# Performance work log

Measured on AMD Instinct MI355X. Metric: run time of the kernel, lower is better.

## Reference

```python
import jax, jax.numpy as jnp
from jax import lax
import numpy as np

B, C_IN, H, W = 4, 3, 128, 128
K, D = 8192, 16  # num_embeddings, embedding_size (= encoder out channels)


def _conv(x, w, b):
    # x: (B,C,H,W), w: (O,I,3,3) OIHW, VALID padding, stride 1
    y = lax.conv_general_dilated(x, w, (1, 1), 'VALID',
                                 dimension_numbers=('NCHW', 'OIHW', 'NCHW'))
    return y + b[None, :, None, None]


def _conv_t(x, w, b):
    # transpose conv, stride 1, k=3: correlate with flipped/transposed kernel, pad 2
    # w: (I,O,3,3) -> flip spatial, swap to OIHW
    wk = jnp.flip(w, (2, 3)).transpose(1, 0, 2, 3)
    y = lax.conv_general_dilated(x, wk, (1, 1), [(2, 2), (2, 2)],
                                 dimension_numbers=('NCHW', 'OIHW', 'NCHW'))
    return y + b[None, :, None, None]


def setup_inputs() -> dict:
    key = jax.random.key(0)
    ks = jax.random.split(key, 14)
    g = lambda k, shp, fan: jax.random.normal(k, shp, jnp.float32) / np.float32(np.sqrt(fan))
    return {
        'x':   jax.random.normal(ks[0], (B, C_IN, H, W), jnp.float32),
        'ew1': g(ks[1], (4, C_IN, 3, 3), C_IN * 9), 'eb1': jnp.zeros((4,), jnp.float32),
        'ew2': g(ks[2], (8, 4, 3, 3), 4 * 9),       'eb2': jnp.zeros((8,), jnp.float32),
        'ew3': g(ks[3], (16, 8, 3, 3), 8 * 9),      'eb3': jnp.zeros((16,), jnp.float32),
        'dw1': g(ks[4], (16, 8, 3, 3), 16 * 9),     'db1': jnp.zeros((8,), jnp.float32),
        'dw2': g(ks[5], (8, 4, 3, 3), 8 * 9),       'db2': jnp.zeros((4,), jnp.float32),
        'dw3': g(ks[6], (4, C_IN, 3, 3), 4 * 9),    'db3': jnp.zeros((C_IN,), jnp.float32),
        'codebook': jax.random.normal(ks[7], (K, D), jnp.float32) * 0.02,
    }


def reference(x, ew1, eb1, ew2, eb2, ew3, eb3, dw1, db1, dw2, db2, dw3, db3, codebook):
    # encode
    z = jax.nn.selu(_conv(x, ew1, eb1))
    z = jax.nn.selu(_conv(z, ew2, eb2))
    z = _conv(z, ew3, eb3)                      # (B, D, h, w)
    b, d, h, w = z.shape
    zf = z.transpose(0, 2, 3, 1).reshape(-1, d)  # (N, D) flattened latents
    # ||z - e||^2 = ||z||^2 - 2 z.e + ||e||^2, argmin over codebook rows
    d2 = ((zf * zf).sum(1, keepdims=True)
          - 2.0 * (zf @ codebook.T)
          + (codebook * codebook).sum(1)[None, :])  # (N, K)
    idx = jnp.argmin(d2, axis=1)                 # (N,) int32
    zq = codebook[idx].reshape(b, h, w, d).transpose(0, 3, 1, 2)  # gather + reshape
    # decode
    y = jax.nn.selu(_conv_t(zq, dw1, db1))
    y = jax.nn.selu(_conv_t(y, dw2, db2))
    y = _conv_t(y, dw3, db3)                     # (B, C_IN, H, W)
    return (y, idx)
```

## Files before the change

### kernel.cpp

```cpp
#include <hip/hip_runtime.h>
#include <math.h>

#define BATCH 4
#define DLAT 16
#define KCB 8192
#define HLAT 122
#define PIX (HLAT*HLAT)
#define NLAT (BATCH*PIX)
#define NT32 (KCB/32)
#define ROWSB 32
#define NVQBLK 1861
#define NWAVE 4
#define TW (NT32/NWAVE)
#define CAPW 1024
#define NCONVBLK 3721

typedef _Float16 half8 __attribute__((ext_vector_type(8)));
typedef float f32x16 __attribute__((ext_vector_type(16)));

__device__ __forceinline__ float selu_np(float x) {
    const float scale = 1.0507009873554805f, alpha = 1.6732632423543772f;
    if (x > 0.f) return __fmul_rn(scale, x);
    return __fmul_rn(scale, __fmul_rn(alpha, expm1f(x)));
}

template<int CI, int CO, int HIN, int WIN, bool DOSELU>
__global__ void conv3x3_np(const float* __restrict__ in, const float* __restrict__ w,
                           const float* __restrict__ bias, float* __restrict__ out) {
    constexpr int HO = HIN - 2, WO = WIN - 2;
    int tid = blockIdx.x * blockDim.x + threadIdx.x;
    constexpr int total = BATCH * CO * HO * WO;
    if (tid >= total) return;
    int j = tid % WO; int t = tid / WO;
    int i = t % HO;   t /= HO;
    int o = t % CO;   int b = t / CO;
    float acc = 0.f;
    for (int c = 0; c < CI; ++c) {
        const float* ip = in + ((b * CI + c) * HIN + i) * WIN + j;
        const float* wp = w + ((o * CI + c) * 3) * 3;
        #pragma unroll
        for (int p = 0; p < 3; ++p)
            #pragma unroll
            for (int q = 0; q < 3; ++q)
                acc = __fmaf_rn(ip[p * WIN + q], wp[p * 3 + q], acc);
    }
    acc = __fadd_rn(acc, bias[o]);
    out[tid] = DOSELU ? selu_np(acc) : acc;
}

__global__ void conv3_last_np(const float* __restrict__ in, const float* __restrict__ w,
                              const float* __restrict__ bias, float* __restrict__ zf,
                              _Float16* __restrict__ zh, float* __restrict__ blockmax) {
    constexpr int CI = 8, HIN = 124, WIN = 124, WO = 122;
    __shared__ float sred[4];
    int tid = blockIdx.x * 256 + threadIdx.x;
    int o  = tid & 15;
    int pp = tid >> 4;
    int b = pp / PIX, pix = pp % PIX;
    int i = pix / WO, j = pix % WO;
    float acc = 0.f;
    for (int c = 0; c < CI; ++c) {
        const float* ip = in + ((b * CI + c) * HIN + i) * WIN + j;
        const float* wp = w + ((o * CI + c) * 3) * 3;
        #pragma unroll
        for (int p = 0; p < 3; ++p)
            #pragma unroll
            for (int q = 0; q < 3; ++q)
                acc = __fmaf_rn(ip[p * WIN + q], wp[p * 3 + q], acc);
    }
    acc = __fadd_rn(acc, bias[o]);
    zf[tid] = acc;
    zh[tid] = (_Float16)acc;
    float m = fabsf(acc);
    #pragma unroll
    for (int off = 32; off; off >>= 1) m = fmaxf(m, __shfl_xor(m, off));
    if ((threadIdx.x & 63) == 0) sred[threadIdx.x >> 6] = m;
    __syncthreads();
    if (threadIdx.x == 0)
        blockmax[blockIdx.x] = fmaxf(fmaxf(sred[0], sred[1]), fmaxf(sred[2], sred[3]));
}

__global__ void reduce_zmax(const float* __restrict__ bm, unsigned* __restrict__ scal) {
    __shared__ float sred[4];
    float m = 0.f;
    for (int i = threadIdx.x; i < NCONVBLK; i += 256) m = fmaxf(m, bm[i]);
    #pragma unroll
    for (int off = 32; off; off >>= 1) m = fmaxf(m, __shfl_xor(m, off));
    if ((threadIdx.x & 63) == 0) sred[threadIdx.x >> 6] = m;
    __syncthreads();
    if (threadIdx.x == 0)
        scal[0] = __float_as_uint(fmaxf(fmaxf(sred[0], sred[1]), fmaxf(sred[2], sred[3])));
}

__device__ __forceinline__ float pairwise16_sq(const float* v) {
    float a[16];
    #pragma unroll
    for (int d = 0; d < 16; ++d) a[d] = __fmul_rn(v[d], v[d]);
    float r0 = __fadd_rn(a[0], a[8]),  r1 = __fadd_rn(a[1], a[9]);
    float r2 = __fadd_rn(a[2], a[10]), r3 = __fadd_rn(a[3], a[11]);
    float r4 = __fadd_rn(a[4], a[12]), r5 = __fadd_rn(a[5], a[13]);
    float r6 = __fadd_rn(a[6], a[14]), r7 = __fadd_rn(a[7], a[15]);
    return __fadd_rn(__fadd_rn(__fadd_rn(r0, r1), __fadd_rn(r2, r3)),
                     __fadd_rn(__fadd_rn(r4, r5), __fadd_rn(r6, r7)));
}

__device__ __forceinline__ void load16(const float* __restrict__ p, float* v) {
    const float4* r = (const float4*)p;
    float4 v0 = r[0], v1 = r[1], v2 = r[2], v3 = r[3];
    v[0]=v0.x; v[1]=v0.y; v[2]=v0.z; v[3]=v0.w;
    v[4]=v1.x; v[5]=v1.y; v[6]=v1.z; v[7]=v1.w;
    v[8]=v2.x; v[9]=v2.y; v[10]=v2.z; v[11]=v2.w;
    v[12]=v3.x; v[13]=v3.y; v[14]=v3.z; v[15]=v3.w;
}

__device__ __forceinline__ float np_d2(const float* zr, float A, const float* e16, float cnk) {
    float g = 0.f;
    #pragma unroll
    for (int d = 0; d < 16; ++d) g = __fmaf_rn(zr[d], e16[d], g);
    return __fadd_rn(__fmaf_rn(-2.f, g, A), cnk);
}

__global__ void init_scal(unsigned* scal) { scal[0] = 0u; scal[1] = 0u; }

__global__ void cbprep(const float* __restrict__ cb, float* __restrict__ cn,
                       _Float16* __restrict__ cbB, unsigned* __restrict__ scal) {
    int k = blockIdx.x * 256 + threadIdx.x;
    float v[16];
    load16(cb + (size_t)k * DLAT, v);
    float C = pairwise16_sq(v);
    cn[k] = C;
    float m = C;
    #pragma unroll
    for (int off = 32; off; off >>= 1) m = fmaxf(m, __shfl_xor(m, off));
    if ((threadIdx.x & 63) == 0) atomicMax(&scal[1], __float_as_uint(m));
    int tile = k >> 5, col = k & 31;
    #pragma unroll
    for (int d = 0; d < 16; ++d) {
        int ln = (d >> 3) * 32 + col;
        cbB[(size_t)tile * 512 + ln * 8 + (d & 7)] = (_Float16)v[d];
    }
}

#define DROW(reg, lanehi) (((reg) & 3) + 8 * ((reg) >> 2) + 4 * (lanehi))

__global__ __launch_bounds__(256, 4) void vq_mfma(
        const _Float16* __restrict__ zh, const float* __restrict__ zf,
        const _Float16* __restrict__ cbB, const float* __restrict__ cn,
        const float* __restrict__ cb, const unsigned* __restrict__ scal,
        float* __restrict__ idx_out, float* __restrict__ zq) {
    __shared__ unsigned list[CAPW];
    __shared__ float resd[CAPW];
    __shared__ float smin[NWAVE][ROWSB];
    __shared__ unsigned lcnt;
    const int tid = threadIdx.x;
    const int w = tid >> 6, lane = tid & 63;
    const int lanehi = lane >> 5;
    const int R0 = blockIdx.x * ROWSB;
    const f32x16 zero16 = {0.f,0.f,0.f,0.f,0.f,0.f,0.f,0.f,0.f,0.f,0.f,0.f,0.f,0.f,0.f,0.f};
    if (tid == 0) lcnt = 0;

    int ar = R0 + (lane & 31);
    if (ar >= NLAT) ar = NLAT - 1;
    half8 a = *(const half8*)(zh + (size_t)ar * DLAT + lanehi * 8);

    float zmaxf = __uint_as_float(scal[0]);
    float en    = sqrtf(__uint_as_float(scal[1]));
    float errG  = 4.f * zmaxf * en * 9.765625e-4f * 1.03f
                + 6.104e-5f * (16.f * zmaxf + 4.f * en);
    float slack = (16.f * zmaxf * zmaxf + 8.f * zmaxf * en + en * en) * 1.2e-7f;
    float DELTA = 4.f * errG + 2.f * slack + 1e-6f;

    const int t0 = w * TW, t1 = t0 + TW;

    float m[16];
    #pragma unroll
    for (int r = 0; r < 16; ++r) m[r] = INFINITY;

    #pragma unroll 2
    for (int t = t0; t < t1; ++t) {
        half8 b = *(const half8*)(cbB + (size_t)t * 512 + lane * 8);
        float cnv = cn[t * 32 + (lane & 31)];
        f32x16 D = __builtin_amdgcn_mfma_f32_32x32x16_f16(a, b, zero16, 0, 0, 0);
        #pragma unroll
        for (int r = 0; r < 16; ++r)
            m[r] = fminf(m[r], __fmaf_rn(-2.f, D[r], cnv));
    }
    #pragma unroll
    for (int r = 0; r < 16; ++r) {
        float v = m[r];
        v = fminf(v, __shfl_xor(v, 1));
        v = fminf(v, __shfl_xor(v, 2));
        v = fminf(v, __shfl_xor(v, 4));
        v = fminf(v, __shfl_xor(v, 8));
        v = fminf(v, __shfl_xor(v, 16));
        m[r] = v;
    }
    if ((lane & 31) == 0) {
        #pragma unroll
        for (int r = 0; r < 16; ++r)
            smin[w][DROW(r, lanehi)] = m[r];
    }
    __syncthreads();
    #pragma unroll
    for (int r = 0; r < 16; ++r) {
        int row = DROW(r, lanehi);
        float v = INFINITY;
        #pragma unroll
        for (int ww = 0; ww < NWAVE; ++ww) v = fminf(v, smin[ww][row]);
        m[r] = v + DELTA;
    }

    #pragma unroll 2
    for (int t = t0; t < t1; ++t) {
        half8 b = *(const half8*)(cbB + (size_t)t * 512 + lane * 8);
        float cnv = cn[t * 32 + (lane & 31)];
        f32x16 D = __builtin_amdgcn_mfma_f32_32x32x16_f16(a, b, zero16, 0, 0, 0);
        bool anyp = false;
        #pragma unroll
        for (int r = 0; r < 16; ++r)
            anyp |= (__fmaf_rn(-2.f, D[r], cnv) <= m[r]);
        if (__ballot(anyp)) {
            #pragma unroll
            for (int r = 0; r < 16; ++r) {
                bool pred = (__fmaf_rn(-2.f, D[r], cnv) <= m[r]);
                unsigned long long bal = __ballot(pred);
                if (bal) {
                    unsigned nb = (unsigned)__popcll(bal);
                    unsigned base = 0;
                    if (lane == 0) base = atomicAdd(&lcnt, nb);
                    base = __shfl(base, 0);
                    unsigned pos = base + (unsigned)__popcll(bal & ((1ull << lane) - 1ull));
                    if (pred && pos < CAPW) {
                        unsigned rs = (unsigned)DROW(r, lanehi);
                        list[pos] = (rs << 13) | (unsigned)(t * 32 + (lane & 31));
                    }
                }
            }
        }
    }
    __syncthreads();
    unsigned cnt = lcnt;

    if (cnt <= CAPW) {
        for (unsigned i = tid; i < cnt; i += 256) {
            unsigned e = list[i];
            int n = R0 + (int)(e >> 13);
            if (n >= NLAT) n = NLAT - 1;
            int k = (int)(e & 8191);
            float zr[16], e16[16];
            load16(zf + (size_t)n * DLAT, zr);
            float A = pairwise16_sq(zr);
            load16(cb + (size_t)k * DLAT, e16);
            resd[i] = np_d2(zr, A, e16, cn[k]);
        }
    }
    __syncthreads();

    if (tid < ROWSB) {
        int r = R0 + tid;
        if (r < NLAT) {
            float bd = INFINITY; int bk = 0x7fffffff;
            if (cnt <= CAPW) {
                for (unsigned i = 0; i < cnt; ++i) {
                    unsigned e = list[i];
                    if ((int)(e >> 13) == tid) {
                        float d2 = resd[i]; int k = (int)(e & 8191);
                        if (d2 < bd || (d2 == bd && k < bk)) { bd = d2; bk = k; }
                    }
                }
            } else {
                float zr[16];
                load16(zf + (size_t)r * DLAT, zr);
                float A = pairwise16_sq(zr);
                for (int k = 0; k < KCB; ++k) {
                    float e16[16];
                    load16(cb + (size_t)k * DLAT, e16);
                    float d2 = np_d2(zr, A, e16, cn[k]);
                    if (d2 < bd) { bd = d2; bk = k; }
                }
            }
            idx_out[r] = (float)bk;
            int b = r / PIX, pix = r % PIX;
            const float* e = cb + (size_t)bk * DLAT;
            #pragma unroll
            for (int d = 0; d < DLAT; ++d) zq[((size_t)(b * DLAT + d)) * PIX + pix] = e[d];
        }
    }
}

template<int CI, int CO, int HIN, int WIN, bool DOSELU>
__global__ void convt3x3(const float* __restrict__ in, const float* __restrict__ w,
                         const float* __restrict__ bias, float* __restrict__ out) {
    constexpr int HO = HIN + 2, WO = WIN + 2;
    int tid = blockIdx.x * blockDim.x + threadIdx.x;
    constexpr int total = BATCH * CO * HO * WO;
    if (tid >= total) return;
    int j = tid % WO; int t = tid / WO;
    int i = t % HO;   t /= HO;
    int o = t % CO;   int b = t / CO;
    float acc = bias[o];
    for (int c = 0; c < CI; ++c) {
        const float* ip = in + ((b * CI + c) * HIN) * WIN;
        const float* wp = w + ((c * CO + o) * 3) * 3;
        #pragma unroll
        for (int p = 0; p < 3; ++p) {
            int ii = i + p - 2;
            if (ii < 0 || ii >= HIN) continue;
            #pragma unroll
            for (int q = 0; q < 3; ++q) {
                int jj = j + q - 2;
                if (jj < 0 || jj >= WIN) continue;
                acc += ip[ii * WIN + jj] * wp[(2 - p) * 3 + (2 - q)];
            }
        }
    }
    const float scale = 1.0507009873554805f, alpha = 1.6732632423543772f;
    out[tid] = DOSELU ? (acc > 0.f ? scale * acc : scale * alpha * (expf(acc) - 1.f)) : acc;
}

extern "C" void kernel_launch(void* const* d_in, const int* in_sizes, int n_in,
                              void* d_out, int out_size, void* d_ws, size_t ws_size,
                              hipStream_t stream) {
    const float* x   = (const float*)d_in[0];
    const float* ew1 = (const float*)d_in[1];  const float* eb1 = (const float*)d_in[2];
    const float* ew2 = (const float*)d_in[3];  const float* eb2 = (const float*)d_in[4];
    const float* ew3 = (const float*)d_in[5];  const float* eb3 = (const float*)d_in[6];
    const float* dw1 = (const float*)d_in[7];  const float* db1 = (const float*)d_in[8];
    const float* dw2 = (const float*)d_in[9];  const float* db2 = (const float*)d_in[10];
    const float* dw3 = (const float*)d_in[11]; const float* db3 = (const float*)d_in[12];
    const float* cb  = (const float*)d_in[13];

    float* out_y   = (float*)d_out;
    float* out_idx = (float*)d_out + 196608;

    float*     ws   = (float*)d_ws;
    float*     zf   = ws;
    float*     e1   = ws + 952576;
    float*     e2   = ws + 1206592;
    float*     fZq  = ws + 952576;
    float*     fB   = ws + 1905152;
    float*     fA   = ws + 2397184;
    _Float16*  zh   = (_Float16*)(ws + 2651200);
    _Float16*  cbB  = (_Float16*)(ws + 3127488);
    float*     cn   = ws + 3193024;
    unsigned*  scal = (unsigned*)(ws + 3201216);
    float*     bmax = ws + 3201218;

    const int TPB = 256;

    init_scal<<<1, 1, 0, stream>>>(scal);

    conv3x3_np<3, 4, 128, 128, true ><<<993,  TPB, 0, stream>>>(x,  ew1, eb1, e1);
    conv3x3_np<4, 8, 126, 126, true ><<<1922, TPB, 0, stream>>>(e1, ew2, eb2, e2);
    conv3_last_np<<<NCONVBLK, TPB, 0, stream>>>(e2, ew3, eb3, zf, zh, bmax);
    reduce_zmax<<<1, TPB, 0, stream>>>(bmax, scal);

    cbprep<<<32, TPB, 0, stream>>>(cb, cn, cbB, scal);
    vq_mfma<<<NVQBLK, TPB, 0, stream>>>(zh, zf, cbB, cn, cb, scal, out_idx, fZq);

    convt3x3<16, 8, 122, 122, true ><<<1922, TPB, 0, stream>>>(fZq, dw1, db1, fB);
    convt3x3<8, 4, 124, 124, true ><<<993,  TPB, 0, stream>>>(fB,  dw2, db2, fA);
    convt3x3<4, 3, 126, 126, false><<<768,  TPB, 0, stream>>>(fA,  dw3, db3, out_y);
}
```

Baseline: 227.1 us.

## Replace second MFMA pass with per-lane minimum candidate rescoring

Drops the second full pass over the codebook that recomputed MFMA distances to gather candidates. Each lane now keeps its own per-row minimum across its strided codebook subset. Lanes whose minimum falls within the row-minimum-plus-DELTA band are recorded in a small per-wave list. For each entry, all 64 lanes rescore the matching codebook column exactly and do a wave argmin reduction. This halves the MFMA work but changes the candidate set: only each lane's own minimum is kept, so other near-ties in that lane's subset may be missed, and any wave overflow falls back to the brute-force path.

New measurement: 287.7 us. 26.7% more time.

```diff
diff --git a/kernel.cpp b/kernel.cpp
--- a/kernel.cpp
+++ b/kernel.cpp
@@ -12,7 +12,8 @@
 #define NVQBLK 1861
 #define NWAVE 4
 #define TW (NT32/NWAVE)
-#define CAPW 1024
+#define CAPW 256
+#define TCAP 64
 #define NCONVBLK 3721
 
 typedef _Float16 half8 __attribute__((ext_vector_type(8)));
@@ -151,6 +152,7 @@
     __shared__ unsigned list[CAPW];
     __shared__ float resd[CAPW];
     __shared__ float smin[NWAVE][ROWSB];
+    __shared__ unsigned tlist[NWAVE][TCAP];
     __shared__ unsigned lcnt;
     const int tid = threadIdx.x;
     const int w = tid >> 6, lane = tid & 63;
@@ -185,6 +187,9 @@
         for (int r = 0; r < 16; ++r)
             m[r] = fminf(m[r], __fmaf_rn(-2.f, D[r], cnv));
     }
+    float mlane[16];
+    #pragma unroll
+    for (int r = 0; r < 16; ++r) mlane[r] = m[r];
     #pragma unroll
     for (int r = 0; r < 16; ++r) {
         float v = m[r];
@@ -210,51 +215,48 @@
         m[r] = v + DELTA;
     }
 
-    #pragma unroll 2
-    for (int t = t0; t < t1; ++t) {
-        half8 b = *(const half8*)(cbB + (size_t)t * 512 + lane * 8);
-        float cnv = cn[t * 32 + (lane & 31)];
-        f32x16 D = __builtin_amdgcn_mfma_f32_32x32x16_f16(a, b, zero16, 0, 0, 0);
-        bool anyp = false;
-        #pragma unroll
-        for (int r = 0; r < 16; ++r)
-            anyp |= (__fmaf_rn(-2.f, D[r], cnv) <= m[r]);
-        if (__ballot(anyp)) {
-            #pragma unroll
-            for (int r = 0; r < 16; ++r) {
-                bool pred = (__fmaf_rn(-2.f, D[r], cnv) <= m[r]);
-                unsigned long long bal = __ballot(pred);
-                if (bal) {
-                    unsigned nb = (unsigned)__popcll(bal);
-                    unsigned base = 0;
-                    if (lane == 0) base = atomicAdd(&lcnt, nb);
-                    base = __shfl(base, 0);
-                    unsigned pos = base + (unsigned)__popcll(bal & ((1ull << lane) - 1ull));
-                    if (pred && pos < CAPW) {
-                        unsigned rs = (unsigned)DROW(r, lanehi);
-                        list[pos] = (rs << 13) | (unsigned)(t * 32 + (lane & 31));
-                    }
-                }
+    unsigned cnt_w = 0;
+    #pragma unroll
+    for (int r = 0; r < 16; ++r) {
+        bool q = (mlane[r] <= m[r]);
+        unsigned long long bal = __ballot(q);
+        if (bal) {
+            unsigned pos = cnt_w + (unsigned)__popcll(bal & ((1ull << lane) - 1ull));
+            if (q && pos < TCAP)
+                tlist[w][pos] = (unsigned)((DROW(r, lanehi) << 5) | (lane & 31));
+            cnt_w += (unsigned)__popcll(bal);
+        }
+    }
+    bool ovf = (cnt_w > TCAP);
+    if (ovf && lane == 0) atomicAdd(&lcnt, CAPW + 1u);
+
+    if (!ovf) {
+        for (unsigned i = 0; i < cnt_w; ++i) {
+            unsigned e = tlist[w][i];
+            int row = (int)(e >> 5), col = (int)(e & 31);
+            int rg = R0 + row; if (rg >= NLAT) rg = NLAT - 1;
+            float zr[16];
+            load16(zf + (size_t)rg * DLAT, zr);
+            float A = pairwise16_sq(zr);
+            int k = (t0 + lane) * 32 + col;
+            float e16[16];
+            load16(cb + (size_t)k * DLAT, e16);
+            float d2 = np_d2(zr, A, e16, cn[k]);
+            int kk = k;
+            #pragma unroll
+            for (int off = 1; off < 64; off <<= 1) {
+                float od = __shfl_xor(d2, off);
+                int   ok = __shfl_xor(kk, off);
+                if (od < d2 || (od == d2 && ok < kk)) { d2 = od; kk = ok; }
+            }
+            if (lane == 0) {
+                unsigned p = atomicAdd(&lcnt, 1u);
+                if (p < CAPW) { list[p] = ((unsigned)row << 13) | (unsigned)kk; resd[p] = d2; }
             }
         }
     }
     __syncthreads();
     unsigned cnt = lcnt;
-
-    if (cnt <= CAPW) {
-        for (unsigned i = tid; i < cnt; i += 256) {
-            unsigned e = list[i];
-            int n = R0 + (int)(e >> 13);
-            if (n >= NLAT) n = NLAT - 1;
-            int k = (int)(e & 8191);
-            float zr[16], e16[16];
-            load16(zf + (size_t)n * DLAT, zr);
-            float A = pairwise16_sq(zr);
-            load16(cb + (size_t)k * DLAT, e16);
-            resd[i] = np_d2(zr, A, e16, cn[k]);
-        }
-    }
-    __syncthreads();
 
     if (tid < ROWSB) {
         int r = R0 + tid;
```

## Stage codebook tiles in LDS with double buffering, 128 rows per VQ block

Applied to the files above, without the earlier changes.

The VQ kernel now gives each wave its own 32 latent rows, so a block covers 128 rows and the grid shrinks about fourfold. Every wave walks the full codebook, which is staged through double-buffered shared memory in chunks of 8 tiles, so each global codebook load is shared by four waves. The cross-wave min reduction in shared memory is gone, and the init_scal launch is folded into reduce_zmax. In exchange each wave does four times as many MFMAs per block, a barrier is added per chunk, occupancy is lowered to 3 blocks per CU, and the 1024-entry candidate list now serves 128 rows instead of 32, so it may overflow into the fallback path more often.

Result: slower. 331.1 us (+45.8%).

```diff
diff --git a/kernel.cpp b/kernel.cpp
--- a/kernel.cpp
+++ b/kernel.cpp
@@ -8,10 +8,11 @@
 #define PIX (HLAT*HLAT)
 #define NLAT (BATCH*PIX)
 #define NT32 (KCB/32)
-#define ROWSB 32
-#define NVQBLK 1861
+#define ROWSB 128
+#define NVQBLK 466
 #define NWAVE 4
-#define TW (NT32/NWAVE)
+#define CHT 8
+#define NCH (NT32/CHT)
 #define CAPW 1024
 #define NCONVBLK 3721
 
@@ -90,6 +91,7 @@
     __syncthreads();
     if (threadIdx.x == 0)
         scal[0] = __float_as_uint(fmaxf(fmaxf(sred[0], sred[1]), fmaxf(sred[2], sred[3])));
+    if (threadIdx.x == 1) scal[1] = 0u;
 }
 
 __device__ __forceinline__ float pairwise16_sq(const float* v) {
@@ -119,8 +121,6 @@
     for (int d = 0; d < 16; ++d) g = __fmaf_rn(zr[d], e16[d], g);
     return __fadd_rn(__fmaf_rn(-2.f, g, A), cnk);
 }
-
-__global__ void init_scal(unsigned* scal) { scal[0] = 0u; scal[1] = 0u; }
 
 __global__ void cbprep(const float* __restrict__ cb, float* __restrict__ cn,
                        _Float16* __restrict__ cbB, unsigned* __restrict__ scal) {
@@ -143,14 +143,14 @@
 
 #define DROW(reg, lanehi) (((reg) & 3) + 8 * ((reg) >> 2) + 4 * (lanehi))
 
-__global__ __launch_bounds__(256, 4) void vq_mfma(
+__global__ __launch_bounds__(256, 3) void vq_mfma(
         const _Float16* __restrict__ zh, const float* __restrict__ zf,
         const _Float16* __restrict__ cbB, const float* __restrict__ cn,
         const float* __restrict__ cb, const unsigned* __restrict__ scal,
         float* __restrict__ idx_out, float* __restrict__ zq) {
+    __shared__ _Float16 sb[2][CHT * 512];
     __shared__ unsigned list[CAPW];
     __shared__ float resd[CAPW];
-    __shared__ float smin[NWAVE][ROWSB];
     __shared__ unsigned lcnt;
     const int tid = threadIdx.x;
     const int w = tid >> 6, lane = tid & 63;
@@ -159,7 +159,7 @@
     const f32x16 zero16 = {0.f,0.f,0.f,0.f,0.f,0.f,0.f,0.f,0.f,0.f,0.f,0.f,0.f,0.f,0.f,0.f};
     if (tid == 0) lcnt = 0;
 
-    int ar = R0 + (lane & 31);
+    int ar = R0 + w * 32 + (lane & 31);
     if (ar >= NLAT) ar = NLAT - 1;
     half8 a = *(const half8*)(zh + (size_t)ar * DLAT + lanehi * 8);
 
@@ -170,71 +170,102 @@
     float slack = (16.f * zmaxf * zmaxf + 8.f * zmaxf * en + en * en) * 1.2e-7f;
     float DELTA = 4.f * errG + 2.f * slack + 1e-6f;
 
-    const int t0 = w * TW, t1 = t0 + TW;
-
-    float m[16];
-    #pragma unroll
-    for (int r = 0; r < 16; ++r) m[r] = INFINITY;
-
-    #pragma unroll 2
-    for (int t = t0; t < t1; ++t) {
-        half8 b = *(const half8*)(cbB + (size_t)t * 512 + lane * 8);
-        float cnv = cn[t * 32 + (lane & 31)];
-        f32x16 D = __builtin_amdgcn_mfma_f32_32x32x16_f16(a, b, zero16, 0, 0, 0);
-        #pragma unroll
-        for (int r = 0; r < 16; ++r)
-            m[r] = fminf(m[r], __fmaf_rn(-2.f, D[r], cnv));
+    const char* src = (const char*)cbB;
+    float4 rg0, rg1;
+
+    float mm[16];
+    #pragma unroll
+    for (int r = 0; r < 16; ++r) mm[r] = INFINITY;
+
+    {
+        rg0 = *(const float4*)(src + tid * 32);
+        rg1 = *(const float4*)(src + tid * 32 + 16);
+        *(float4*)((char*)&sb[0][0] + tid * 32) = rg0;
+        *(float4*)((char*)&sb[0][0] + tid * 32 + 16) = rg1;
+        int cur = 0;
+        for (int c = 0; c < NCH; ++c) {
+            if (c + 1 < NCH) {
+                const char* s2 = src + (size_t)(c + 1) * (CHT * 1024);
+                rg0 = *(const float4*)(s2 + tid * 32);
+                rg1 = *(const float4*)(s2 + tid * 32 + 16);
+            }
+            __syncthreads();
+            #pragma unroll
+            for (int tt = 0; tt < CHT; ++tt) {
+                half8 b = *(const half8*)&sb[cur][tt * 512 + lane * 8];
+                float cnv = cn[(c * CHT + tt) * 32 + (lane & 31)];
+                f32x16 D = __builtin_amdgcn_mfma_f32_32x32x16_f16(a, b, zero16, 0, 0, 0);
+                #pragma unroll
+                for (int r = 0; r < 16; ++r)
+                    mm[r] = fminf(mm[r], __fmaf_rn(-2.f, D[r], cnv));
+            }
+            if (c + 1 < NCH) {
+                int nxt = cur ^ 1;
+                *(float4*)((char*)&sb[nxt][0] + tid * 32) = rg0;
+                *(float4*)((char*)&sb[nxt][0] + tid * 32 + 16) = rg1;
+                cur = nxt;
+            }
+        }
     }
     #pragma unroll
     for (int r = 0; r < 16; ++r) {
-        float v = m[r];
+        float v = mm[r];
         v = fminf(v, __shfl_xor(v, 1));
         v = fminf(v, __shfl_xor(v, 2));
         v = fminf(v, __shfl_xor(v, 4));
         v = fminf(v, __shfl_xor(v, 8));
         v = fminf(v, __shfl_xor(v, 16));
-        m[r] = v;
-    }
-    if ((lane & 31) == 0) {
-        #pragma unroll
-        for (int r = 0; r < 16; ++r)
-            smin[w][DROW(r, lanehi)] = m[r];
-    }
-    __syncthreads();
-    #pragma unroll
-    for (int r = 0; r < 16; ++r) {
-        int row = DROW(r, lanehi);
-        float v = INFINITY;
-        #pragma unroll
-        for (int ww = 0; ww < NWAVE; ++ww) v = fminf(v, smin[ww][row]);
-        m[r] = v + DELTA;
-    }
-
-    #pragma unroll 2
-    for (int t = t0; t < t1; ++t) {
-        half8 b = *(const half8*)(cbB + (size_t)t * 512 + lane * 8);
-        float cnv = cn[t * 32 + (lane & 31)];
-        f32x16 D = __builtin_amdgcn_mfma_f32_32x32x16_f16(a, b, zero16, 0, 0, 0);
-        bool anyp = false;
-        #pragma unroll
-        for (int r = 0; r < 16; ++r)
-            anyp |= (__fmaf_rn(-2.f, D[r], cnv) <= m[r]);
-        if (__ballot(anyp)) {
-            #pragma unroll
-            for (int r = 0; r < 16; ++r) {
-                bool pred = (__fmaf_rn(-2.f, D[r], cnv) <= m[r]);
-                unsigned long long bal = __ballot(pred);
-                if (bal) {
-                    unsigned nb = (unsigned)__popcll(bal);
-                    unsigned base = 0;
-                    if (lane == 0) base = atomicAdd(&lcnt, nb);
-                    base = __shfl(base, 0);
-                    unsigned pos = base + (unsigned)__popcll(bal & ((1ull << lane) - 1ull));
-                    if (pred && pos < CAPW) {
-                        unsigned rs = (unsigned)DROW(r, lanehi);
-                        list[pos] = (rs << 13) | (unsigned)(t * 32 + (lane & 31));
+        mm[r] = v + DELTA;
+    }
+    __syncthreads();
+
+    {
+        rg0 = *(const float4*)(src + tid * 32);
+        rg1 = *(const float4*)(src + tid * 32 + 16);
+        *(float4*)((char*)&sb[0][0] + tid * 32) = rg0;
+        *(float4*)((char*)&sb[0][0] + tid * 32 + 16) = rg1;
+        int cur = 0;
+        for (int c = 0; c < NCH; ++c) {
+            if (c + 1 < NCH) {
+                const char* s2 = src + (size_t)(c + 1) * (CHT * 1024);
+                rg0 = *(const float4*)(s2 + tid * 32);
+                rg1 = *(const float4*)(s2 + tid * 32 + 16);
+            }
+            __syncthreads();
+            #pragma unroll
+            for (int tt = 0; tt < CHT; ++tt) {
+                half8 b = *(const half8*)&sb[cur][tt * 512 + lane * 8];
+                int t = c * CHT + tt;
+                float cnv = cn[t * 32 + (lane & 31)];
+                f32x16 D = __builtin_amdgcn_mfma_f32_32x32x16_f16(a, b, zero16, 0, 0, 0);
+                bool anyp = false;
+                #pragma unroll
+                for (int r = 0; r < 16; ++r)
+                    anyp |= (__fmaf_rn(-2.f, D[r], cnv) <= mm[r]);
+                if (__ballot(anyp)) {
+                    #pragma unroll
+                    for (int r = 0; r < 16; ++r) {
+                        bool pred = (__fmaf_rn(-2.f, D[r], cnv) <= mm[r]);
+                        unsigned long long bal = __ballot(pred);
+                        if (bal) {
+                            unsigned nb = (unsigned)__popcll(bal);
+                            unsigned base = 0;
+                            if (lane == 0) base = atomicAdd(&lcnt, nb);
+                            base = __shfl(base, 0);
+                            unsigned pos = base + (unsigned)__popcll(bal & ((1ull << lane) - 1ull));
+                            if (pred && pos < CAPW) {
+                                unsigned rs = (unsigned)(w * 32 + DROW(r, lanehi));
+                                list[pos] = (rs << 13) | (unsigned)(t * 32 + (lane & 31));
+                            }
+                        }
                     }
                 }
+            }
+            if (c + 1 < NCH) {
+                int nxt = cur ^ 1;
+                *(float4*)((char*)&sb[nxt][0] + tid * 32) = rg0;
+                *(float4*)((char*)&sb[nxt][0] + tid * 32 + 16) = rg1;
+                cur = nxt;
             }
         }
     }
@@ -348,8 +379,6 @@
 
     const int TPB = 256;
 
-    init_scal<<<1, 1, 0, stream>>>(scal);
-
     conv3x3_np<3, 4, 128, 128, true ><<<993,  TPB, 0, stream>>>(x,  ew1, eb1, e1);
     conv3x3_np<4, 8, 126, 126, true ><<<1922, TPB, 0, stream>>>(e1, ew2, eb2, e2);
     conv3_last_np<<<NCONVBLK, TPB, 0, stream>>>(e2, ew3, eb3, zf, zh, bmax);
```
